# Kernel tuning notes

Measured on AMD Instinct MI355X. Metric: run time of the kernel, lower is better.

The kernel has to match this reference:

```python
import jax, jax.numpy as jnp
from jax import lax
import numpy as np

EPS = 0.15      # constraint_value_upper_bound (per-row box |y/c - 1| <= EPS)
DELTA = 0.05    # groups_constraint_upper_bound (per-group mean |y/c - 1| <= DELTA)
N_GROUPS = 8
N_ITERS = 300   # Dykstra iterations; converges to the exact QP projection

N, D, H1, H2, K = 65536, 512, 1024, 512, 1


def setup_inputs() -> dict:
    key = jax.random.key(0)
    ks = jax.random.split(key, 8)
    x = jax.random.normal(ks[0], (N, D), jnp.float32)
    W1 = jax.random.normal(ks[1], (D, H1), jnp.float32) / np.float32(np.sqrt(D))
    b1 = jnp.zeros((H1,), jnp.float32)
    W2 = jax.random.normal(ks[2], (H1, H2), jnp.float32) / np.float32(np.sqrt(H1))
    b2 = jnp.zeros((H2,), jnp.float32)
    Wf = jax.random.normal(ks[3], (H2, K), jnp.float32) / np.float32(np.sqrt(H2))
    bf = jnp.zeros((K,), jnp.float32)
    c = jax.random.uniform(ks[4], (N,), jnp.float32, 0.5, 2.0)
    # quantiles_price_tensor: q_i = (1/N) * #{k : c_k <= c_i}  (rank via searchsorted)
    q = jnp.searchsorted(jnp.sort(c), c, side='right').astype(jnp.float32) / N
    # group j covers q in [j/G, (j+1)/G]; assign boundary ties to the lower group
    g = jnp.clip(jnp.ceil(q * N_GROUPS).astype(jnp.int32) - 1, 0, N_GROUPS - 1)
    group_mask = jax.nn.one_hot(g, N_GROUPS, dtype=jnp.float32).T  # [G, N]
    return dict(x=x, W1=W1, b1=b1, W2=W2, b2=b2, Wf=Wf, bf=bf,
                constraint_constant=c, group_mask=group_mask)


def _project(y_u, c, group_mask):
    """Exact QP: min ||y - y_u||^2 s.t. |y_i/c_i - 1| <= EPS and
    |mean_{i in G_j}(y_i/c_i - 1)| <= DELTA, solved by Dykstra's alternating
    projections in z = y/c - 1 space under the weighted norm sum c_i^2 z_i^2."""
    w = c * c                                   # [N] weights of the norm
    z0 = y_u / c[:, None] - 1.0                 # [N, K]
    n = group_mask.sum(axis=1)                  # [G] group sizes
    a = group_mask / n[:, None]                 # [G, N] averaging rows
    denom = (a * a / w[None, :]).sum(axis=1)    # [G]  a^T W^{-1} a
    u = (a / w[None, :]) / denom[:, None]       # [G, N] weighted slab directions

    def proj_box(z):
        return jnp.clip(z, -EPS, EPS)

    def proj_grp(z):
        v = a @ z                               # [G, K] group means
        return z - u.T @ (v - jnp.clip(v, -DELTA, DELTA))

    def body(carry, _):
        z, p, q = carry
        zb = proj_box(z + p); p = z + p - zb
        zg = proj_grp(zb + q); q = zb + q - zg
        return (zg, p, q), None

    init = (z0, jnp.zeros_like(z0), jnp.zeros_like(z0))
    (z, _, _), _ = lax.scan(body, init, None, length=N_ITERS)
    return (z + 1.0) * c[:, None]


def reference(x, W1, b1, W2, b2, Wf, bf, constraint_constant, group_mask):
    h = jax.nn.relu(x @ W1 + b1)   # Dropout is identity in eval mode
    h = jax.nn.relu(h @ W2 + b2)
    y_u = h @ Wf + bf              # [N, 1] unconstrained predictions
    return _project(y_u, constraint_constant, group_mask)
```

## Files before the change

### kernel.cpp

```cpp
#include <hip/hip_runtime.h>
#include <hip/hip_bf16.h>

#define NROWS 65536
#define DIM   512
#define H1DIM 1024
#define H2DIM 512
#define EPSC  0.15f
#define DELTA 0.05f
#define NGRP  8
#define CAPG  16384

typedef __bf16 bf16x8 __attribute__((ext_vector_type(8)));
typedef float  f32x4  __attribute__((ext_vector_type(4)));

__device__ __forceinline__ void gload16(const void* g, void* lds) {
  __builtin_amdgcn_global_load_lds((__attribute__((address_space(1))) const unsigned int*)g,
                                   (__attribute__((address_space(3))) unsigned int*)lds,
                                   16, 0, 0);
}

__global__ void k_zero(float* y_u, int n, int* cnt) {
  int i = blockIdx.x * blockDim.x + threadIdx.x;
  if (i < n) y_u[i] = 0.f;
  if (i < NGRP) cnt[i] = 0;
}

__global__ void k_tcvt(const float* __restrict__ src, __bf16* __restrict__ dst, int R, int C) {
  __shared__ float tile[32][33];
  const int bi = blockIdx.x * 32;
  const int bj = blockIdx.y * 32;
  const int tx = threadIdx.x, ty = threadIdx.y;
  #pragma unroll
  for (int r = ty; r < 32; r += 8)
    tile[r][tx] = src[(size_t)(bi + r) * C + bj + tx];
  __syncthreads();
  #pragma unroll
  for (int r = ty; r < 32; r += 8)
    dst[(size_t)(bj + r) * R + bi + tx] = (__bf16)tile[tx][r];
}

__global__ __launch_bounds__(256) void k_cvt_x(const float4* __restrict__ x4,
                                               bf16x8* __restrict__ xb8, int n8) {
  int i = blockIdx.x * blockDim.x + threadIdx.x;
  const int stride = gridDim.x * blockDim.x;
  for (; i < n8; i += stride) {
    const float4 a = x4[2 * i];
    const float4 b = x4[2 * i + 1];
    bf16x8 v;
    v[0] = (__bf16)a.x; v[1] = (__bf16)a.y; v[2] = (__bf16)a.z; v[3] = (__bf16)a.w;
    v[4] = (__bf16)b.x; v[5] = (__bf16)b.y; v[6] = (__bf16)b.z; v[7] = (__bf16)b.w;
    xb8[i] = v;
  }
}


__global__ __launch_bounds__(512, 2) void k_gemm1(const __bf16* __restrict__ xb,
                                                  const __bf16* __restrict__ w1t,
                                                  const float* __restrict__ b1,
                                                  __bf16* __restrict__ h1) {
  __shared__ __align__(16) __bf16 As[2][256 * 64];
  __shared__ __align__(16) __bf16 Bs[2][256 * 64];
  const int tid = threadIdx.x;
  const int w = tid >> 6, l = tid & 63;
  const int mt   = (int)gridDim.x >> 2;
  const int mper = mt >> 3;
  const int xcd  = blockIdx.x & 7;
  const int idx  = blockIdx.x >> 3;
  const int brow = (xcd * mper + (idx >> 2)) * 256;
  const int bcol = (idx & 3) * 256;
  const int lr = l & 15, lk = l >> 4;
  const int wm = w >> 2, wn = w & 3;
  const int mbase = wm * 128, nbase = wn * 64;
  const int srow = w * 32 + (l >> 3);
  const int scol = (((l & 7) ^ ((l >> 3) & 7)) * 8);
  const int swz  = (lr & 7) << 4;
  const int NT = DIM / 64;
  f32x4 acc[8][4] = {};

  #define STAGE1(KT, BUF) do { \
    _Pragma("unroll") for (int t_ = 0; t_ < 4; ++t_) { \
      gload16(xb  + (size_t)(brow + srow + t_ * 8) * DIM + (KT) + scol, \
              As[BUF] + (w * 32 + t_ * 8) * 64); \
      gload16(w1t + (size_t)(bcol + srow + t_ * 8) * DIM + (KT) + scol, \
              Bs[BUF] + (w * 32 + t_ * 8) * 64); } } while (0)
  #define COMPUTE1(BUF) do { \
    _Pragma("unroll") for (int kk = 0; kk < 64; kk += 32) { \
      bf16x8 af[8], bq[4]; \
      _Pragma("unroll") for (int m = 0; m < 8; ++m) \
        af[m] = *(const bf16x8*)((const char*)(As[BUF]) + \
                 ((((mbase + m * 16 + lr) * 128) + kk * 2 + lk * 16) ^ swz)); \
      _Pragma("unroll") for (int nn = 0; nn < 4; ++nn) \
        bq[nn] = *(const bf16x8*)((const char*)(Bs[BUF]) + \
                 ((((nbase + nn * 16 + lr) * 128) + kk * 2 + lk * 16) ^ swz)); \
      __builtin_amdgcn_s_setprio(1); \
      _Pragma("unroll") for (int m = 0; m < 8; ++m) \
        _Pragma("unroll") for (int nn = 0; nn < 4; ++nn) \
          acc[m][nn] = __builtin_amdgcn_mfma_f32_16x16x32_bf16(af[m], bq[nn], acc[m][nn], 0, 0, 0); \
      __builtin_amdgcn_s_setprio(0); \
    } } while (0)

  STAGE1(0, 0);
  int cur = 0;
  for (int t = 0; t < NT - 1; ++t) {
    STAGE1((t + 1) * 64, cur ^ 1);
    asm volatile("s_waitcnt vmcnt(8)" ::: "memory");
    __builtin_amdgcn_s_barrier();
    COMPUTE1(cur);
    __builtin_amdgcn_s_barrier();
    cur ^= 1;
  }
  asm volatile("s_waitcnt vmcnt(0)" ::: "memory");
  __builtin_amdgcn_s_barrier();
  COMPUTE1(cur);

  #undef STAGE1
  #undef COMPUTE1

  #pragma unroll
  for (int nn = 0; nn < 4; ++nn) {
    const int col = bcol + nbase + nn * 16 + lr;
    const float bias = b1[col];
    #pragma unroll
    for (int m = 0; m < 8; ++m) {
      const int row = brow + mbase + m * 16 + lk * 4;
      #pragma unroll
      for (int j = 0; j < 4; ++j) {
        float v = acc[m][nn][j] + bias;
        v = fmaxf(v, 0.f);
        h1[(size_t)(row + j) * H1DIM + col] = (__bf16)v;
      }
    }
  }
}

__global__ __launch_bounds__(512, 2) void k_gemm2(const __bf16* __restrict__ h1,
                                                  const __bf16* __restrict__ w2t,
                                                  const float* __restrict__ b2,
                                                  const float* __restrict__ wf,
                                                  float* __restrict__ y_u, int row0) {
  __shared__ __align__(16) __bf16 As[2][256 * 64];
  __shared__ __align__(16) __bf16 Bs[2][256 * 64];
  __shared__ float yred[256];
  const int tid = threadIdx.x;
  const int w = tid >> 6, l = tid & 63;
  const int mt   = (int)gridDim.x >> 1;
  const int mper = mt >> 3;
  const int xcd  = blockIdx.x & 7;
  const int idx  = blockIdx.x >> 3;
  const int brow = (xcd * mper + (idx >> 1)) * 256;
  const int n0   = (idx & 1) * 256;
  const int lr = l & 15, lk = l >> 4;
  const int wm = w >> 2, wn = w & 3;
  const int mbase = wm * 128, nbase = wn * 64;
  const int srow = w * 32 + (l >> 3);
  const int scol = (((l & 7) ^ ((l >> 3) & 7)) * 8);
  const int swz  = (lr & 7) << 4;
  const int NT = H1DIM / 64;
  f32x4 acc[8][4] = {};

  #define STAGE2(KT, BUF) do { \
    _Pragma("unroll") for (int t_ = 0; t_ < 4; ++t_) { \
      gload16(h1  + (size_t)(brow + srow + t_ * 8) * H1DIM + (KT) + scol, \
              As[BUF] + (w * 32 + t_ * 8) * 64); \
      gload16(w2t + (size_t)(n0   + srow + t_ * 8) * H1DIM + (KT) + scol, \
              Bs[BUF] + (w * 32 + t_ * 8) * 64); } } while (0)
  #define COMPUTE2(BUF) do { \
    _Pragma("unroll") for (int kk = 0; kk < 64; kk += 32) { \
      bf16x8 af[8], bq[4]; \
      _Pragma("unroll") for (int m = 0; m < 8; ++m) \
        af[m] = *(const bf16x8*)((const char*)(As[BUF]) + \
                 ((((mbase + m * 16 + lr) * 128) + kk * 2 + lk * 16) ^ swz)); \
      _Pragma("unroll") for (int nn = 0; nn < 4; ++nn) \
        bq[nn] = *(const bf16x8*)((const char*)(Bs[BUF]) + \
                 ((((nbase + nn * 16 + lr) * 128) + kk * 2 + lk * 16) ^ swz)); \
      __builtin_amdgcn_s_setprio(1); \
      _Pragma("unroll") for (int m = 0; m < 8; ++m) \
        _Pragma("unroll") for (int nn = 0; nn < 4; ++nn) \
          acc[m][nn] = __builtin_amdgcn_mfma_f32_16x16x32_bf16(af[m], bq[nn], acc[m][nn], 0, 0, 0); \
      __builtin_amdgcn_s_setprio(0); \
    } } while (0)

  STAGE2(0, 0);
  int cur = 0;
  for (int t = 0; t < NT - 1; ++t) {
    STAGE2((t + 1) * 64, cur ^ 1);
    asm volatile("s_waitcnt vmcnt(8)" ::: "memory");
    __builtin_amdgcn_s_barrier();
    COMPUTE2(cur);
    __builtin_amdgcn_s_barrier();
    cur ^= 1;
  }
  asm volatile("s_waitcnt vmcnt(0)" ::: "memory");
  __builtin_amdgcn_s_barrier();
  COMPUTE2(cur);

  #undef STAGE2
  #undef COMPUTE2

  float yacc[8][4] = {};
  #pragma unroll
  for (int nn = 0; nn < 4; ++nn) {
    const int col = n0 + nbase + nn * 16 + lr;
    const float bias = b2[col];
    const float wfv = wf[col];
    #pragma unroll
    for (int m = 0; m < 8; ++m)
      #pragma unroll
      for (int j = 0; j < 4; ++j)
        yacc[m][j] += fmaxf(acc[m][nn][j] + bias, 0.f) * wfv;
  }
  #pragma unroll
  for (int m = 0; m < 8; ++m)
    #pragma unroll
    for (int j = 0; j < 4; ++j) {
      float v = yacc[m][j];
      v += __shfl_xor(v, 1, 64);
      v += __shfl_xor(v, 2, 64);
      v += __shfl_xor(v, 4, 64);
      v += __shfl_xor(v, 8, 64);
      yacc[m][j] = v;
    }
  if (tid < 256) yred[tid] = 0.f;
  __syncthreads();
  if (lr == 0) {
    #pragma unroll
    for (int m = 0; m < 8; ++m)
      #pragma unroll
      for (int j = 0; j < 4; ++j)
        atomicAdd(&yred[mbase + m * 16 + lk * 4 + j], yacc[m][j]);
  }
  __syncthreads();
  if (tid < 256) atomicAdd(&y_u[row0 + brow + tid], yred[tid]);
}

__global__ __launch_bounds__(256) void k_scatter(const float* __restrict__ y_u,
                                                 const float* __restrict__ c,
                                                 const float* __restrict__ mask,
                                                 const float* __restrict__ bfp,
                                                 float* __restrict__ z0c, float* __restrict__ wc,
                                                 unsigned char* __restrict__ gidx,
                                                 int* __restrict__ cnt, int n) {
  __shared__ int lcnt[NGRP];
  __shared__ int lbase[NGRP];
  const float bf0 = bfp[0];
  const int tid = threadIdx.x;
  if (tid < NGRP) lcnt[tid] = 0;
  __syncthreads();
  const int i = blockIdx.x * blockDim.x + tid;
  int g = 0, slot_l = 0;
  float z0 = 0.f, wv = 0.f;
  if (i < n) {
    const float cv = c[i];
    z0 = (y_u[i] + bf0) / cv - 1.f;
    wv = cv * cv;
    #pragma unroll
    for (int j = 1; j < NGRP; ++j)
      if (mask[(size_t)j * NROWS + i] > 0.5f) g = j;
    slot_l = atomicAdd(&lcnt[g], 1);
    gidx[i] = (unsigned char)g;
  }
  __syncthreads();
  if (tid < NGRP) lbase[tid] = atomicAdd(&cnt[tid], lcnt[tid]);
  __syncthreads();
  if (i < n) {
    const int slot = lbase[g] + slot_l;
    if (slot < CAPG) {
      z0c[(size_t)g * CAPG + slot] = z0;
      wc [(size_t)g * CAPG + slot] = wv;
    }
  }
}

__device__ __forceinline__ float wave_red(float v, int mode) {
  #pragma unroll
  for (int o = 32; o > 0; o >>= 1) {
    float u = __shfl_xor(v, o, 64);
    v = (mode == 0) ? (v + u) : ((mode == 1) ? fmaxf(v, u) : fminf(v, u));
  }
  return v;
}
__device__ __forceinline__ float block_red(float v, int mode, float* red, int tid) {
  v = wave_red(v, mode);
  if ((tid & 63) == 0) red[tid >> 6] = v;
  __syncthreads();
  if (tid < 64) {
    float x = (tid < 16) ? red[tid] : (mode == 0 ? 0.f : (mode == 1 ? -1e30f : 1e30f));
    x = wave_red(x, mode);
    if (tid == 0) red[0] = x;
  }
  __syncthreads();
  float r = red[0];
  __syncthreads();
  return r;
}

__global__ __launch_bounds__(1024) void k_mu(const float* __restrict__ z0c,
                                             const float* __restrict__ wc,
                                             const int* __restrict__ cnt,
                                             float* __restrict__ muarr) {
  __shared__ float red[16];
  const int g = blockIdx.x;
  const int tid = threadIdx.x;
  int n = cnt[g];
  if (n > CAPG) n = CAPG;
  if (n <= 0) { if (tid == 0) muarr[g] = 0.f; return; }
  float z0v[16], iwv[16];
  float hmax = -1e30f, hmin = 1e30f;
  #pragma unroll
  for (int t = 0; t < 16; ++t) {
    const int idx = t * 1024 + tid;
    if (idx < n) {
      const float z0 = z0c[(size_t)g * CAPG + idx];
      const float wv = wc[(size_t)g * CAPG + idx];
      z0v[t] = z0; iwv[t] = 1.f / wv;
      hmax = fmaxf(hmax, (z0 + EPSC) * wv);
      hmin = fminf(hmin, (z0 - EPSC) * wv);
    } else { z0v[t] = 0.f; iwv[t] = 0.f; }
  }
  const float inv_n = 1.f / (float)n;
  #define EVALM(MU, OUT) do { float s_ = 0.f; \
    _Pragma("unroll") for (int t = 0; t < 16; ++t) \
      s_ += fminf(fmaxf(z0v[t] - (MU) * iwv[t], -EPSC), EPSC); \
    OUT = block_red(s_, 0, red, tid) * inv_n; } while (0)
  float m0; EVALM(0.f, m0);
  float mu = 0.f;
  if (fabsf(m0) > DELTA) {
    float target, lo, hi;
    if (m0 > 0.f) { target = DELTA;  lo = 0.f; hi = block_red(hmax, 1, red, tid); }
    else          { target = -DELTA; hi = 0.f; lo = block_red(hmin, 2, red, tid); }
    for (int it = 0; it < 32; ++it) {
      const float mid = 0.5f * (lo + hi);
      float mm; EVALM(mid, mm);
      if (mm >= target) lo = mid; else hi = mid;
    }
    mu = 0.5f * (lo + hi);
  }
  if (tid == 0) muarr[g] = mu;
  #undef EVALM
}

__global__ void k_y(const float* __restrict__ y_u, const float* __restrict__ c,
                    const float* __restrict__ bfp, const unsigned char* __restrict__ gidx,
                    const float* __restrict__ muarr, float* __restrict__ out, int n) {
  const float bf0 = bfp[0];
  int i = blockIdx.x * blockDim.x + threadIdx.x;
  const int stride = gridDim.x * blockDim.x;
  for (; i < n; i += stride) {
    const float cv = c[i];
    const float z0 = (y_u[i] + bf0) / cv - 1.f;
    const float wv = cv * cv;
    const float mu = muarr[gidx[i]];
    const float z = fminf(fmaxf(z0 - mu / wv, -EPSC), EPSC);
    out[i] = (z + 1.f) * cv;
  }
}

extern "C" void kernel_launch(void* const* d_in, const int* in_sizes, int n_in,
                              void* d_out, int out_size, void* d_ws, size_t ws_size,
                              hipStream_t stream) {
  const float* x    = (const float*)d_in[0];
  const float* W1   = (const float*)d_in[1];
  const float* b1   = (const float*)d_in[2];
  const float* W2   = (const float*)d_in[3];
  const float* b2   = (const float*)d_in[4];
  const float* Wf   = (const float*)d_in[5];
  const float* bfp  = (const float*)d_in[6];
  const float* c    = (const float*)d_in[7];
  const float* mask = (const float*)d_in[8];
  float* out = (float*)d_out;

  char* ws = (char*)d_ws;
  size_t off = 0;
  auto alloc = [&](size_t bytes) -> void* {
    void* p = ws + off;
    off += (bytes + 255) & ~(size_t)255;
    return p;
  };
  __bf16* w1t = (__bf16*)alloc((size_t)H1DIM * DIM * 2);
  __bf16* w2t = (__bf16*)alloc((size_t)H2DIM * H1DIM * 2);
  float* y_u  = (float*)alloc((size_t)NROWS * 4);
  float* z0c  = (float*)alloc((size_t)NGRP * CAPG * 4);
  float* wc   = (float*)alloc((size_t)NGRP * CAPG * 4);
  unsigned char* gidx = (unsigned char*)alloc(NROWS);
  int*   cnt  = (int*)alloc(NGRP * 4);
  float* muarr = (float*)alloc(NGRP * 4);
  const size_t fixed = off;

  size_t avail = (ws_size > fixed) ? (ws_size - fixed) : 0;
  long long rc = (long long)(avail / ((size_t)(DIM + H1DIM * 2)));
  rc &= ~2047LL;
  if (rc > 32768) rc = 32768;
  if (rc < 2048) rc = 2048;
  const int rows_chunk = (int)rc;
  __bf16* xb = (__bf16*)(ws + fixed);
  __bf16* h1 = (__bf16*)(ws + fixed + (size_t)rows_chunk * DIM * 2);

  k_zero<<<dim3((NROWS + 255) / 256), dim3(256), 0, stream>>>(y_u, NROWS, cnt);
  k_tcvt<<<dim3(DIM / 32, H1DIM / 32), dim3(32, 8), 0, stream>>>(W1, w1t, DIM, H1DIM);
  k_tcvt<<<dim3(H1DIM / 32, H2DIM / 32), dim3(32, 8), 0, stream>>>(W2, w2t, H1DIM, H2DIM);

  for (int r0 = 0; r0 < NROWS; r0 += rows_chunk) {
    const int Mc = (NROWS - r0 < rows_chunk) ? (NROWS - r0) : rows_chunk;
    const int mtiles = Mc / 256;
    const int n8 = Mc * (DIM / 8);
    int cblocks = (n8 + 255) / 256; if (cblocks > 2048) cblocks = 2048;
    k_cvt_x<<<dim3(cblocks), dim3(256), 0, stream>>>(
        (const float4*)(x + (size_t)r0 * DIM), (bf16x8*)xb, n8);
    k_gemm1<<<dim3(mtiles * 4), dim3(512), 0, stream>>>(xb, w1t, b1, h1);
    k_gemm2<<<dim3(mtiles * 2), dim3(512), 0, stream>>>(h1, w2t, b2, Wf, y_u, r0);
  }

  k_scatter<<<dim3((NROWS + 255) / 256), dim3(256), 0, stream>>>(y_u, c, mask, bfp, z0c, wc, gidx, cnt, NROWS);
  k_mu<<<dim3(NGRP), dim3(1024), 0, stream>>>(z0c, wc, cnt, muarr);
  k_y<<<dim3(256), dim3(256), 0, stream>>>(y_u, c, bfp, gidx, muarr, out, NROWS);
}
```

Before: 242.0 us.

## Split GEMM k-tile compute into barrier-separated quadrant phases for LDS/MFMA interleave

Both GEMM kernels' per-k-tile compute is restructured into four quadrant phases: A and B fragments are read from LDS in halves and MFMAs run on 2x2 quadrants of the accumulator tile, with block barriers between phases. The goal is to stagger waves so that, with two blocks per CU, one wave's LDS reads overlap another's MFMA bursts, and to lower peak fragment-register pressure. In exchange it adds eight barriers per k-tile, which may serialize waves and add stall overhead. The loop is also restructured so the final tile runs inside the loop.

```diff
diff --git a/kernel.cpp b/kernel.cpp
--- a/kernel.cpp
+++ b/kernel.cpp
@@ -53,6 +53,44 @@
   }
 }
 
+
+#define RD_A(LDSA, MH) do { \
+  _Pragma("unroll") for (int kk_ = 0; kk_ < 2; ++kk_) \
+    _Pragma("unroll") for (int m_ = 0; m_ < 4; ++m_) \
+      aR[kk_][m_] = *(const bf16x8*)((const char*)(LDSA) + \
+        ((((mbase + (MH) * 64 + m_ * 16 + lr) * 128) + kk_ * 64 + lk * 16) ^ swz)); \
+} while (0)
+#define RD_B(LDSB, NH) do { \
+  _Pragma("unroll") for (int kk_ = 0; kk_ < 2; ++kk_) \
+    _Pragma("unroll") for (int j_ = 0; j_ < 2; ++j_) \
+      bR[NH][kk_][j_] = *(const bf16x8*)((const char*)(LDSB) + \
+        ((((nbase + (NH) * 32 + j_ * 16 + lr) * 128) + kk_ * 64 + lk * 16) ^ swz)); \
+} while (0)
+#define MFMA_Q(MH, NH) do { \
+  __builtin_amdgcn_s_setprio(1); \
+  _Pragma("unroll") for (int kk_ = 0; kk_ < 2; ++kk_) \
+    _Pragma("unroll") for (int m_ = 0; m_ < 4; ++m_) \
+      _Pragma("unroll") for (int j_ = 0; j_ < 2; ++j_) \
+        acc[(MH) * 4 + m_][(NH) * 2 + j_] = __builtin_amdgcn_mfma_f32_16x16x32_bf16( \
+            aR[kk_][m_], bR[NH][kk_][j_], acc[(MH) * 4 + m_][(NH) * 2 + j_], 0, 0, 0); \
+  __builtin_amdgcn_s_setprio(0); \
+} while (0)
+#define KTILE_PHASES(BUFA, BUFB) do { \
+  RD_A(BUFA, 0); RD_B(BUFB, 0); \
+  __builtin_amdgcn_s_barrier(); \
+  MFMA_Q(0, 0); \
+  __builtin_amdgcn_s_barrier(); \
+  RD_B(BUFB, 1); \
+  __builtin_amdgcn_s_barrier(); \
+  MFMA_Q(0, 1); \
+  __builtin_amdgcn_s_barrier(); \
+  RD_A(BUFA, 1); \
+  __builtin_amdgcn_s_barrier(); \
+  MFMA_Q(1, 1); \
+  __builtin_amdgcn_s_barrier(); \
+  MFMA_Q(1, 0); \
+  __builtin_amdgcn_s_barrier(); \
+} while (0)
 
 __global__ __launch_bounds__(512, 2) void k_gemm1(const __bf16* __restrict__ xb,
                                                   const __bf16* __restrict__ w1t,
@@ -76,6 +114,8 @@
   const int swz  = (lr & 7) << 4;
   const int NT = DIM / 64;
   f32x4 acc[8][4] = {};
+  bf16x8 aR[2][4];
+  bf16x8 bR[2][2][2];
 
   #define STAGE1(KT, BUF) do { \
     _Pragma("unroll") for (int t_ = 0; t_ < 4; ++t_) { \
@@ -83,38 +123,21 @@
               As[BUF] + (w * 32 + t_ * 8) * 64); \
       gload16(w1t + (size_t)(bcol + srow + t_ * 8) * DIM + (KT) + scol, \
               Bs[BUF] + (w * 32 + t_ * 8) * 64); } } while (0)
-  #define COMPUTE1(BUF) do { \
-    _Pragma("unroll") for (int kk = 0; kk < 64; kk += 32) { \
-      bf16x8 af[8], bq[4]; \
-      _Pragma("unroll") for (int m = 0; m < 8; ++m) \
-        af[m] = *(const bf16x8*)((const char*)(As[BUF]) + \
-                 ((((mbase + m * 16 + lr) * 128) + kk * 2 + lk * 16) ^ swz)); \
-      _Pragma("unroll") for (int nn = 0; nn < 4; ++nn) \
-        bq[nn] = *(const bf16x8*)((const char*)(Bs[BUF]) + \
-                 ((((nbase + nn * 16 + lr) * 128) + kk * 2 + lk * 16) ^ swz)); \
-      __builtin_amdgcn_s_setprio(1); \
-      _Pragma("unroll") for (int m = 0; m < 8; ++m) \
-        _Pragma("unroll") for (int nn = 0; nn < 4; ++nn) \
-          acc[m][nn] = __builtin_amdgcn_mfma_f32_16x16x32_bf16(af[m], bq[nn], acc[m][nn], 0, 0, 0); \
-      __builtin_amdgcn_s_setprio(0); \
-    } } while (0)
 
   STAGE1(0, 0);
   int cur = 0;
-  for (int t = 0; t < NT - 1; ++t) {
-    STAGE1((t + 1) * 64, cur ^ 1);
-    asm volatile("s_waitcnt vmcnt(8)" ::: "memory");
+  for (int t = 0; t < NT; ++t) {
+    if (t + 1 < NT) {
+      STAGE1((t + 1) * 64, cur ^ 1);
+      asm volatile("s_waitcnt vmcnt(8)" ::: "memory");
+    } else {
+      asm volatile("s_waitcnt vmcnt(0)" ::: "memory");
+    }
     __builtin_amdgcn_s_barrier();
-    COMPUTE1(cur);
-    __builtin_amdgcn_s_barrier();
+    KTILE_PHASES(As[cur], Bs[cur]);
     cur ^= 1;
   }
-  asm volatile("s_waitcnt vmcnt(0)" ::: "memory");
-  __builtin_amdgcn_s_barrier();
-  COMPUTE1(cur);
-
   #undef STAGE1
-  #undef COMPUTE1
 
   #pragma unroll
   for (int nn = 0; nn < 4; ++nn) {
@@ -157,6 +180,8 @@
   const int swz  = (lr & 7) << 4;
   const int NT = H1DIM / 64;
   f32x4 acc[8][4] = {};
+  bf16x8 aR[2][4];
+  bf16x8 bR[2][2][2];
 
   #define STAGE2(KT, BUF) do { \
     _Pragma("unroll") for (int t_ = 0; t_ < 4; ++t_) { \
@@ -164,38 +189,21 @@
               As[BUF] + (w * 32 + t_ * 8) * 64); \
       gload16(w2t + (size_t)(n0   + srow + t_ * 8) * H1DIM + (KT) + scol, \
               Bs[BUF] + (w * 32 + t_ * 8) * 64); } } while (0)
-  #define COMPUTE2(BUF) do { \
-    _Pragma("unroll") for (int kk = 0; kk < 64; kk += 32) { \
-      bf16x8 af[8], bq[4]; \
-      _Pragma("unroll") for (int m = 0; m < 8; ++m) \
-        af[m] = *(const bf16x8*)((const char*)(As[BUF]) + \
-                 ((((mbase + m * 16 + lr) * 128) + kk * 2 + lk * 16) ^ swz)); \
-      _Pragma("unroll") for (int nn = 0; nn < 4; ++nn) \
-        bq[nn] = *(const bf16x8*)((const char*)(Bs[BUF]) + \
-                 ((((nbase + nn * 16 + lr) * 128) + kk * 2 + lk * 16) ^ swz)); \
-      __builtin_amdgcn_s_setprio(1); \
-      _Pragma("unroll") for (int m = 0; m < 8; ++m) \
-        _Pragma("unroll") for (int nn = 0; nn < 4; ++nn) \
-          acc[m][nn] = __builtin_amdgcn_mfma_f32_16x16x32_bf16(af[m], bq[nn], acc[m][nn], 0, 0, 0); \
-      __builtin_amdgcn_s_setprio(0); \
-    } } while (0)
 
   STAGE2(0, 0);
   int cur = 0;
-  for (int t = 0; t < NT - 1; ++t) {
-    STAGE2((t + 1) * 64, cur ^ 1);
-    asm volatile("s_waitcnt vmcnt(8)" ::: "memory");
+  for (int t = 0; t < NT; ++t) {
+    if (t + 1 < NT) {
+      STAGE2((t + 1) * 64, cur ^ 1);
+      asm volatile("s_waitcnt vmcnt(8)" ::: "memory");
+    } else {
+      asm volatile("s_waitcnt vmcnt(0)" ::: "memory");
+    }
     __builtin_amdgcn_s_barrier();
-    COMPUTE2(cur);
-    __builtin_amdgcn_s_barrier();
+    KTILE_PHASES(As[cur], Bs[cur]);
     cur ^= 1;
   }
-  asm volatile("s_waitcnt vmcnt(0)" ::: "memory");
-  __builtin_amdgcn_s_barrier();
-  COMPUTE2(cur);
-
   #undef STAGE2
-  #undef COMPUTE2
 
   float yacc[8][4] = {};
   #pragma unroll
```

After: 256.1 us. 5.9% more time.

## Fuse projection tail into one per-group kernel with Newton-bisection solve

Applied to the files above, without the earlier changes.

Replaces the scatter, mu-solve and output kernels with a single per-group kernel. It compacts each group's rows into LDS with a ballot-based scan, solves for the group's dual multiplier with a safeguarded Newton step in 12 iterations instead of 32 bisection steps, and writes the outputs directly. The y_u zeroing moves into the first conversion kernel, which removes one more launch. The cost is a serial read of the full mask row by only 8 blocks, plus an LDS capacity cap of 10240 rows per group.

```diff
diff --git a/kernel.cpp b/kernel.cpp
--- a/kernel.cpp
+++ b/kernel.cpp
@@ -8,7 +8,7 @@
 #define EPSC  0.15f
 #define DELTA 0.05f
 #define NGRP  8
-#define CAPG  16384
+#define PCAP  10240
 
 typedef __bf16 bf16x8 __attribute__((ext_vector_type(8)));
 typedef float  f32x4  __attribute__((ext_vector_type(4)));
@@ -17,12 +17,6 @@
   __builtin_amdgcn_global_load_lds((__attribute__((address_space(1))) const unsigned int*)g,
                                    (__attribute__((address_space(3))) unsigned int*)lds,
                                    16, 0, 0);
-}
-
-__global__ void k_zero(float* y_u, int n, int* cnt) {
-  int i = blockIdx.x * blockDim.x + threadIdx.x;
-  if (i < n) y_u[i] = 0.f;
-  if (i < NGRP) cnt[i] = 0;
 }
 
 __global__ void k_tcvt(const float* __restrict__ src, __bf16* __restrict__ dst, int R, int C) {
@@ -40,10 +34,10 @@
 }
 
 __global__ __launch_bounds__(256) void k_cvt_x(const float4* __restrict__ x4,
-                                               bf16x8* __restrict__ xb8, int n8) {
-  int i = blockIdx.x * blockDim.x + threadIdx.x;
+                                               bf16x8* __restrict__ xb8, int n8,
+                                               float* __restrict__ y_u, int zn) {
   const int stride = gridDim.x * blockDim.x;
-  for (; i < n8; i += stride) {
+  for (int i = blockIdx.x * blockDim.x + threadIdx.x; i < n8; i += stride) {
     const float4 a = x4[2 * i];
     const float4 b = x4[2 * i + 1];
     bf16x8 v;
@@ -51,6 +45,8 @@
     v[4] = (__bf16)b.x; v[5] = (__bf16)b.y; v[6] = (__bf16)b.z; v[7] = (__bf16)b.w;
     xb8[i] = v;
   }
+  for (int j = blockIdx.x * blockDim.x + threadIdx.x; j < zn; j += stride)
+    y_u[j] = 0.f;
 }
 
 
@@ -233,126 +229,134 @@
   if (tid < 256) atomicAdd(&y_u[row0 + brow + tid], yred[tid]);
 }
 
-__global__ __launch_bounds__(256) void k_scatter(const float* __restrict__ y_u,
-                                                 const float* __restrict__ c,
-                                                 const float* __restrict__ mask,
-                                                 const float* __restrict__ bfp,
-                                                 float* __restrict__ z0c, float* __restrict__ wc,
-                                                 unsigned char* __restrict__ gidx,
-                                                 int* __restrict__ cnt, int n) {
-  __shared__ int lcnt[NGRP];
-  __shared__ int lbase[NGRP];
-  const float bf0 = bfp[0];
-  const int tid = threadIdx.x;
-  if (tid < NGRP) lcnt[tid] = 0;
-  __syncthreads();
-  const int i = blockIdx.x * blockDim.x + tid;
-  int g = 0, slot_l = 0;
-  float z0 = 0.f, wv = 0.f;
-  if (i < n) {
-    const float cv = c[i];
-    z0 = (y_u[i] + bf0) / cv - 1.f;
-    wv = cv * cv;
-    #pragma unroll
-    for (int j = 1; j < NGRP; ++j)
-      if (mask[(size_t)j * NROWS + i] > 0.5f) g = j;
-    slot_l = atomicAdd(&lcnt[g], 1);
-    gidx[i] = (unsigned char)g;
-  }
-  __syncthreads();
-  if (tid < NGRP) lbase[tid] = atomicAdd(&cnt[tid], lcnt[tid]);
-  __syncthreads();
-  if (i < n) {
-    const int slot = lbase[g] + slot_l;
-    if (slot < CAPG) {
-      z0c[(size_t)g * CAPG + slot] = z0;
-      wc [(size_t)g * CAPG + slot] = wv;
-    }
-  }
-}
-
-__device__ __forceinline__ float wave_red(float v, int mode) {
-  #pragma unroll
-  for (int o = 32; o > 0; o >>= 1) {
-    float u = __shfl_xor(v, o, 64);
-    v = (mode == 0) ? (v + u) : ((mode == 1) ? fmaxf(v, u) : fminf(v, u));
-  }
-  return v;
-}
-__device__ __forceinline__ float block_red(float v, int mode, float* red, int tid) {
-  v = wave_red(v, mode);
-  if ((tid & 63) == 0) red[tid >> 6] = v;
-  __syncthreads();
-  if (tid < 64) {
-    float x = (tid < 16) ? red[tid] : (mode == 0 ? 0.f : (mode == 1 ? -1e30f : 1e30f));
-    x = wave_red(x, mode);
-    if (tid == 0) red[0] = x;
-  }
-  __syncthreads();
-  float r = red[0];
-  __syncthreads();
-  return r;
-}
-
-__global__ __launch_bounds__(1024) void k_mu(const float* __restrict__ z0c,
-                                             const float* __restrict__ wc,
-                                             const int* __restrict__ cnt,
-                                             float* __restrict__ muarr) {
-  __shared__ float red[16];
+__global__ __launch_bounds__(1024) void k_proj(const float* __restrict__ y_u,
+                                               const float* __restrict__ c,
+                                               const float* __restrict__ mask,
+                                               const float* __restrict__ bfp,
+                                               float* __restrict__ out) {
+  __shared__ float z0s[PCAP];
+  __shared__ float iws[PCAP];
+  __shared__ int   idxs[PCAP];
+  __shared__ float reds[16], redd[16];
+  __shared__ int   gcount;
   const int g = blockIdx.x;
   const int tid = threadIdx.x;
-  int n = cnt[g];
-  if (n > CAPG) n = CAPG;
-  if (n <= 0) { if (tid == 0) muarr[g] = 0.f; return; }
-  float z0v[16], iwv[16];
+  const int lane = tid & 63;
+  const int wid = tid >> 6;
+  const float bf0 = bfp[0];
+  if (tid == 0) gcount = 0;
+  __syncthreads();
+  for (int i = tid; i < NROWS; i += 1024) {
+    const bool in = mask[(size_t)g * NROWS + i] > 0.5f;
+    const unsigned long long b = __ballot(in);
+    const int pre = __popcll(b & ((1ull << lane) - 1));
+    int wbase = 0;
+    if (lane == 0 && b) wbase = atomicAdd(&gcount, __popcll(b));
+    wbase = __shfl(wbase, 0, 64);
+    if (in) {
+      const int s = wbase + pre;
+      if (s < PCAP) {
+        const float cv = c[i];
+        z0s[s]  = (y_u[i] + bf0) / cv - 1.f;
+        iws[s]  = 1.f / (cv * cv);
+        idxs[s] = i;
+      }
+    }
+  }
+  __syncthreads();
+  int n = gcount; if (n > PCAP) n = PCAP;
+  const float inv_n = (n > 0) ? 1.f / (float)n : 0.f;
+  float z0v[10], iwv[10];
   float hmax = -1e30f, hmin = 1e30f;
   #pragma unroll
-  for (int t = 0; t < 16; ++t) {
-    const int idx = t * 1024 + tid;
-    if (idx < n) {
-      const float z0 = z0c[(size_t)g * CAPG + idx];
-      const float wv = wc[(size_t)g * CAPG + idx];
-      z0v[t] = z0; iwv[t] = 1.f / wv;
-      hmax = fmaxf(hmax, (z0 + EPSC) * wv);
-      hmin = fminf(hmin, (z0 - EPSC) * wv);
+  for (int t = 0; t < 10; ++t) {
+    const int s = t * 1024 + tid;
+    if (s < n) {
+      z0v[t] = z0s[s]; iwv[t] = iws[s];
+      const float wv = 1.f / iwv[t];
+      hmax = fmaxf(hmax, (z0v[t] + EPSC) * wv);
+      hmin = fminf(hmin, (z0v[t] - EPSC) * wv);
     } else { z0v[t] = 0.f; iwv[t] = 0.f; }
   }
-  const float inv_n = 1.f / (float)n;
-  #define EVALM(MU, OUT) do { float s_ = 0.f; \
-    _Pragma("unroll") for (int t = 0; t < 16; ++t) \
-      s_ += fminf(fmaxf(z0v[t] - (MU) * iwv[t], -EPSC), EPSC); \
-    OUT = block_red(s_, 0, red, tid) * inv_n; } while (0)
-  float m0; EVALM(0.f, m0);
+  #define RED2(SV, DV) do { \
+    _Pragma("unroll") for (int o_ = 32; o_ > 0; o_ >>= 1) { \
+      SV += __shfl_xor(SV, o_, 64); DV += __shfl_xor(DV, o_, 64); } \
+    if (lane == 0) { reds[wid] = SV; redd[wid] = DV; } \
+    __syncthreads(); \
+    if (tid < 64) { \
+      float a_ = (tid < 16) ? reds[tid] : 0.f; \
+      float b_ = (tid < 16) ? redd[tid] : 0.f; \
+      _Pragma("unroll") for (int o_ = 32; o_ > 0; o_ >>= 1) { \
+        a_ += __shfl_xor(a_, o_, 64); b_ += __shfl_xor(b_, o_, 64); } \
+      if (tid == 0) { reds[0] = a_; redd[0] = b_; } \
+    } \
+    __syncthreads(); \
+    SV = reds[0]; DV = redd[0]; \
+    __syncthreads(); \
+  } while (0)
+  #define EVAL2(MU, MS, DS) do { \
+    float s_ = 0.f, d_ = 0.f; \
+    _Pragma("unroll") for (int t_ = 0; t_ < 10; ++t_) { \
+      float zz_ = z0v[t_] - (MU) * iwv[t_]; \
+      if (zz_ > EPSC) zz_ = EPSC; \
+      else if (zz_ < -EPSC) zz_ = -EPSC; \
+      else d_ += iwv[t_]; \
+      s_ += zz_; } \
+    RED2(s_, d_); \
+    MS = s_ * inv_n; DS = d_ * inv_n; \
+  } while (0)
   float mu = 0.f;
-  if (fabsf(m0) > DELTA) {
-    float target, lo, hi;
-    if (m0 > 0.f) { target = DELTA;  lo = 0.f; hi = block_red(hmax, 1, red, tid); }
-    else          { target = -DELTA; hi = 0.f; lo = block_red(hmin, 2, red, tid); }
-    for (int it = 0; it < 32; ++it) {
-      const float mid = 0.5f * (lo + hi);
-      float mm; EVALM(mid, mm);
-      if (mm >= target) lo = mid; else hi = mid;
+  if (n > 0) {
+    float m0, d0;
+    EVAL2(0.f, m0, d0);
+    if (fabsf(m0) > DELTA) {
+      float hx = hmax, hn = -hmin;
+      #pragma unroll
+      for (int o_ = 32; o_ > 0; o_ >>= 1) {
+        hx = fmaxf(hx, __shfl_xor(hx, o_, 64));
+        hn = fmaxf(hn, __shfl_xor(hn, o_, 64));
+      }
+      if (lane == 0) { reds[wid] = hx; redd[wid] = hn; }
+      __syncthreads();
+      if (tid < 64) {
+        float a_ = (tid < 16) ? reds[tid] : -1e30f;
+        float b_ = (tid < 16) ? redd[tid] : -1e30f;
+        #pragma unroll
+        for (int o_ = 32; o_ > 0; o_ >>= 1) {
+          a_ = fmaxf(a_, __shfl_xor(a_, o_, 64));
+          b_ = fmaxf(b_, __shfl_xor(b_, o_, 64));
+        }
+        if (tid == 0) { reds[0] = a_; redd[0] = b_; }
+      }
+      __syncthreads();
+      const float hmax_r = reds[0], hmin_r = -redd[0];
+      __syncthreads();
+      float target, lo, hi;
+      if (m0 > 0.f) { target = DELTA;  lo = 0.f;     hi = hmax_r; }
+      else          { target = -DELTA; lo = hmin_r;  hi = 0.f;    }
+      mu = 0.5f * (lo + hi);
+      for (int it = 0; it < 12; ++it) {
+        float mm, dd;
+        EVAL2(mu, mm, dd);
+        if (mm >= target) lo = mu; else hi = mu;
+        float nm = (dd > 0.f) ? mu + (mm - target) / dd : 0.5f * (lo + hi);
+        if (!(nm > lo && nm < hi)) nm = 0.5f * (lo + hi);
+        mu = nm;
+      }
     }
-    mu = 0.5f * (lo + hi);
-  }
-  if (tid == 0) muarr[g] = mu;
-  #undef EVALM
-}
-
-__global__ void k_y(const float* __restrict__ y_u, const float* __restrict__ c,
-                    const float* __restrict__ bfp, const unsigned char* __restrict__ gidx,
-                    const float* __restrict__ muarr, float* __restrict__ out, int n) {
-  const float bf0 = bfp[0];
-  int i = blockIdx.x * blockDim.x + threadIdx.x;
-  const int stride = gridDim.x * blockDim.x;
-  for (; i < n; i += stride) {
-    const float cv = c[i];
-    const float z0 = (y_u[i] + bf0) / cv - 1.f;
-    const float wv = cv * cv;
-    const float mu = muarr[gidx[i]];
-    const float z = fminf(fmaxf(z0 - mu / wv, -EPSC), EPSC);
-    out[i] = (z + 1.f) * cv;
-  }
+  }
+  #pragma unroll
+  for (int t = 0; t < 10; ++t) {
+    const int s = t * 1024 + tid;
+    if (s < n) {
+      float z = z0v[t] - mu * iwv[t];
+      z = fminf(fmaxf(z, -EPSC), EPSC);
+      const int ri = idxs[s];
+      out[ri] = (z + 1.f) * c[ri];
+    }
+  }
+  #undef RED2
+  #undef EVAL2
 }
 
 extern "C" void kernel_launch(void* const* d_in, const int* in_sizes, int n_in,
@@ -379,15 +383,10 @@
   __bf16* w1t = (__bf16*)alloc((size_t)H1DIM * DIM * 2);
   __bf16* w2t = (__bf16*)alloc((size_t)H2DIM * H1DIM * 2);
   float* y_u  = (float*)alloc((size_t)NROWS * 4);
-  float* z0c  = (float*)alloc((size_t)NGRP * CAPG * 4);
-  float* wc   = (float*)alloc((size_t)NGRP * CAPG * 4);
-  unsigned char* gidx = (unsigned char*)alloc(NROWS);
-  int*   cnt  = (int*)alloc(NGRP * 4);
-  float* muarr = (float*)alloc(NGRP * 4);
   const size_t fixed = off;
 
   size_t avail = (ws_size > fixed) ? (ws_size - fixed) : 0;
-  long long rc = (long long)(avail / ((size_t)(DIM + H1DIM * 2)));
+  long long rc = (long long)(avail / ((size_t)(DIM * 2 + H1DIM * 2)));
   rc &= ~2047LL;
   if (rc > 32768) rc = 32768;
   if (rc < 2048) rc = 2048;
@@ -395,22 +394,22 @@
   __bf16* xb = (__bf16*)(ws + fixed);
   __bf16* h1 = (__bf16*)(ws + fixed + (size_t)rows_chunk * DIM * 2);
 
-  k_zero<<<dim3((NROWS + 255) / 256), dim3(256), 0, stream>>>(y_u, NROWS, cnt);
   k_tcvt<<<dim3(DIM / 32, H1DIM / 32), dim3(32, 8), 0, stream>>>(W1, w1t, DIM, H1DIM);
   k_tcvt<<<dim3(H1DIM / 32, H2DIM / 32), dim3(32, 8), 0, stream>>>(W2, w2t, H1DIM, H2DIM);
 
+  bool first = true;
   for (int r0 = 0; r0 < NROWS; r0 += rows_chunk) {
     const int Mc = (NROWS - r0 < rows_chunk) ? (NROWS - r0) : rows_chunk;
     const int mtiles = Mc / 256;
     const int n8 = Mc * (DIM / 8);
     int cblocks = (n8 + 255) / 256; if (cblocks > 2048) cblocks = 2048;
     k_cvt_x<<<dim3(cblocks), dim3(256), 0, stream>>>(
-        (const float4*)(x + (size_t)r0 * DIM), (bf16x8*)xb, n8);
+        (const float4*)(x + (size_t)r0 * DIM), (bf16x8*)xb, n8,
+        y_u, first ? NROWS : 0);
+    first = false;
     k_gemm1<<<dim3(mtiles * 4), dim3(512), 0, stream>>>(xb, w1t, b1, h1);
     k_gemm2<<<dim3(mtiles * 2), dim3(512), 0, stream>>>(h1, w2t, b2, Wf, y_u, r0);
   }
 
-  k_scatter<<<dim3((NROWS + 255) / 256), dim3(256), 0, stream>>>(y_u, c, mask, bfp, z0c, wc, gidx, cnt, NROWS);
-  k_mu<<<dim3(NGRP), dim3(1024), 0, stream>>>(z0c, wc, cnt, muarr);
-  k_y<<<dim3(256), dim3(256), 0, stream>>>(y_u, c, bfp, gidx, muarr, out, NROWS);
-}
+  k_proj<<<dim3(NGRP), dim3(1024), 0, stream>>>(y_u, c, mask, bfp, out);
+}
```

After: 279.9 us. 15.7% more time.

## Replace bisection for group multiplier with safeguarded Newton and fuse zero-init

Applied to the files above, without the earlier changes.

The per-group dual multiplier search in k_mu drops 32 bisection steps in favour of about 12 safeguarded Newton steps. Each step reduces the clipped sum and its derivative (the sum of inverse weights over unclipped entries) together in one paired block reduction, and the two max/min bound reductions are merged into one pass. This is meant to cut the serial chain of block-wide reductions and barriers in a kernel that runs only 8 blocks. The separate zeroing kernel is folded into the first k_cvt_x launch, and inverse weights are stored precomputed. The workspace chunk sizing formula also changes, which may give fewer, smaller row chunks, and Newton accuracy relies on the bisection fallback.

```diff
diff --git a/kernel.cpp b/kernel.cpp
--- a/kernel.cpp
+++ b/kernel.cpp
@@ -19,12 +19,6 @@
                                    16, 0, 0);
 }
 
-__global__ void k_zero(float* y_u, int n, int* cnt) {
-  int i = blockIdx.x * blockDim.x + threadIdx.x;
-  if (i < n) y_u[i] = 0.f;
-  if (i < NGRP) cnt[i] = 0;
-}
-
 __global__ void k_tcvt(const float* __restrict__ src, __bf16* __restrict__ dst, int R, int C) {
   __shared__ float tile[32][33];
   const int bi = blockIdx.x * 32;
@@ -40,10 +34,12 @@
 }
 
 __global__ __launch_bounds__(256) void k_cvt_x(const float4* __restrict__ x4,
-                                               bf16x8* __restrict__ xb8, int n8) {
-  int i = blockIdx.x * blockDim.x + threadIdx.x;
+                                               bf16x8* __restrict__ xb8, int n8,
+                                               float* __restrict__ y_u, int zn,
+                                               int* __restrict__ cnt) {
   const int stride = gridDim.x * blockDim.x;
-  for (; i < n8; i += stride) {
+  const int tid0 = blockIdx.x * blockDim.x + threadIdx.x;
+  for (int i = tid0; i < n8; i += stride) {
     const float4 a = x4[2 * i];
     const float4 b = x4[2 * i + 1];
     bf16x8 v;
@@ -51,6 +47,8 @@
     v[4] = (__bf16)b.x; v[5] = (__bf16)b.y; v[6] = (__bf16)b.z; v[7] = (__bf16)b.w;
     xb8[i] = v;
   }
+  for (int j = tid0; j < zn; j += stride) y_u[j] = 0.f;
+  if (zn > 0 && tid0 < NGRP) cnt[tid0] = 0;
 }
 
 
@@ -237,7 +235,7 @@
                                                  const float* __restrict__ c,
                                                  const float* __restrict__ mask,
                                                  const float* __restrict__ bfp,
-                                                 float* __restrict__ z0c, float* __restrict__ wc,
+                                                 float* __restrict__ z0c, float* __restrict__ iwc,
                                                  unsigned char* __restrict__ gidx,
                                                  int* __restrict__ cnt, int n) {
   __shared__ int lcnt[NGRP];
@@ -248,11 +246,11 @@
   __syncthreads();
   const int i = blockIdx.x * blockDim.x + tid;
   int g = 0, slot_l = 0;
-  float z0 = 0.f, wv = 0.f;
+  float z0 = 0.f, iw = 0.f;
   if (i < n) {
     const float cv = c[i];
     z0 = (y_u[i] + bf0) / cv - 1.f;
-    wv = cv * cv;
+    iw = 1.f / (cv * cv);
     #pragma unroll
     for (int j = 1; j < NGRP; ++j)
       if (mask[(size_t)j * NROWS + i] > 0.5f) g = j;
@@ -266,39 +264,39 @@
     const int slot = lbase[g] + slot_l;
     if (slot < CAPG) {
       z0c[(size_t)g * CAPG + slot] = z0;
-      wc [(size_t)g * CAPG + slot] = wv;
-    }
-  }
-}
-
-__device__ __forceinline__ float wave_red(float v, int mode) {
+      iwc[(size_t)g * CAPG + slot] = iw;
+    }
+  }
+}
+
+__device__ __forceinline__ void red2(float& a, float& b, float* reda, float* redb, int tid) {
   #pragma unroll
   for (int o = 32; o > 0; o >>= 1) {
-    float u = __shfl_xor(v, o, 64);
-    v = (mode == 0) ? (v + u) : ((mode == 1) ? fmaxf(v, u) : fminf(v, u));
-  }
-  return v;
-}
-__device__ __forceinline__ float block_red(float v, int mode, float* red, int tid) {
-  v = wave_red(v, mode);
-  if ((tid & 63) == 0) red[tid >> 6] = v;
+    a += __shfl_xor(a, o, 64);
+    b += __shfl_xor(b, o, 64);
+  }
+  if ((tid & 63) == 0) { reda[tid >> 6] = a; redb[tid >> 6] = b; }
   __syncthreads();
   if (tid < 64) {
-    float x = (tid < 16) ? red[tid] : (mode == 0 ? 0.f : (mode == 1 ? -1e30f : 1e30f));
-    x = wave_red(x, mode);
-    if (tid == 0) red[0] = x;
-  }
-  __syncthreads();
-  float r = red[0];
-  __syncthreads();
-  return r;
+    float x = (tid < 16) ? reda[tid] : 0.f;
+    float y = (tid < 16) ? redb[tid] : 0.f;
+    #pragma unroll
+    for (int o = 32; o > 0; o >>= 1) {
+      x += __shfl_xor(x, o, 64);
+      y += __shfl_xor(y, o, 64);
+    }
+    if (tid == 0) { reda[0] = x; redb[0] = y; }
+  }
+  __syncthreads();
+  a = reda[0]; b = redb[0];
+  __syncthreads();
 }
 
 __global__ __launch_bounds__(1024) void k_mu(const float* __restrict__ z0c,
-                                             const float* __restrict__ wc,
+                                             const float* __restrict__ iwc,
                                              const int* __restrict__ cnt,
                                              float* __restrict__ muarr) {
-  __shared__ float red[16];
+  __shared__ float reda[16], redb[16];
   const int g = blockIdx.x;
   const int tid = threadIdx.x;
   int n = cnt[g];
@@ -311,32 +309,66 @@
     const int idx = t * 1024 + tid;
     if (idx < n) {
       const float z0 = z0c[(size_t)g * CAPG + idx];
-      const float wv = wc[(size_t)g * CAPG + idx];
-      z0v[t] = z0; iwv[t] = 1.f / wv;
+      const float iw = iwc[(size_t)g * CAPG + idx];
+      z0v[t] = z0; iwv[t] = iw;
+      const float wv = 1.f / iw;
       hmax = fmaxf(hmax, (z0 + EPSC) * wv);
       hmin = fminf(hmin, (z0 - EPSC) * wv);
     } else { z0v[t] = 0.f; iwv[t] = 0.f; }
   }
   const float inv_n = 1.f / (float)n;
-  #define EVALM(MU, OUT) do { float s_ = 0.f; \
-    _Pragma("unroll") for (int t = 0; t < 16; ++t) \
-      s_ += fminf(fmaxf(z0v[t] - (MU) * iwv[t], -EPSC), EPSC); \
-    OUT = block_red(s_, 0, red, tid) * inv_n; } while (0)
-  float m0; EVALM(0.f, m0);
+  #define EVAL2(MU, MS, DS) do { \
+    float s_ = 0.f, d_ = 0.f; \
+    _Pragma("unroll") for (int t_ = 0; t_ < 16; ++t_) { \
+      float zz_ = z0v[t_] - (MU) * iwv[t_]; \
+      if (zz_ > EPSC) zz_ = EPSC; \
+      else if (zz_ < -EPSC) zz_ = -EPSC; \
+      else d_ += iwv[t_]; \
+      s_ += zz_; } \
+    red2(s_, d_, reda, redb, tid); \
+    MS = s_ * inv_n; DS = d_ * inv_n; \
+  } while (0)
+  float m0, d0;
+  EVAL2(0.f, m0, d0);
   float mu = 0.f;
   if (fabsf(m0) > DELTA) {
+    float hx = hmax, hn = -hmin;
+    #pragma unroll
+    for (int o = 32; o > 0; o >>= 1) {
+      hx = fmaxf(hx, __shfl_xor(hx, o, 64));
+      hn = fmaxf(hn, __shfl_xor(hn, o, 64));
+    }
+    if ((tid & 63) == 0) { reda[tid >> 6] = hx; redb[tid >> 6] = hn; }
+    __syncthreads();
+    if (tid < 64) {
+      float x = (tid < 16) ? reda[tid] : -1e30f;
+      float y = (tid < 16) ? redb[tid] : -1e30f;
+      #pragma unroll
+      for (int o = 32; o > 0; o >>= 1) {
+        x = fmaxf(x, __shfl_xor(x, o, 64));
+        y = fmaxf(y, __shfl_xor(y, o, 64));
+      }
+      if (tid == 0) { reda[0] = x; redb[0] = y; }
+    }
+    __syncthreads();
+    const float hmax_r = reda[0], hmin_r = -redb[0];
+    __syncthreads();
     float target, lo, hi;
-    if (m0 > 0.f) { target = DELTA;  lo = 0.f; hi = block_red(hmax, 1, red, tid); }
-    else          { target = -DELTA; hi = 0.f; lo = block_red(hmin, 2, red, tid); }
-    for (int it = 0; it < 32; ++it) {
-      const float mid = 0.5f * (lo + hi);
-      float mm; EVALM(mid, mm);
-      if (mm >= target) lo = mid; else hi = mid;
-    }
-    mu = 0.5f * (lo + hi);
+    if (m0 > 0.f) { target = DELTA;  lo = 0.f;    hi = hmax_r; }
+    else          { target = -DELTA; lo = hmin_r; hi = 0.f;    }
+    mu = (d0 > 0.f) ? (m0 - target) / d0 : 0.5f * (lo + hi);
+    if (!(mu > lo && mu < hi)) mu = 0.5f * (lo + hi);
+    for (int it = 0; it < 12; ++it) {
+      float mm, dd;
+      EVAL2(mu, mm, dd);
+      if (mm >= target) lo = mu; else hi = mu;
+      float nm = (dd > 0.f) ? mu + (mm - target) / dd : 0.5f * (lo + hi);
+      if (!(nm > lo && nm < hi)) nm = 0.5f * (lo + hi);
+      mu = nm;
+    }
   }
   if (tid == 0) muarr[g] = mu;
-  #undef EVALM
+  #undef EVAL2
 }
 
 __global__ void k_y(const float* __restrict__ y_u, const float* __restrict__ c,
@@ -348,9 +380,8 @@
   for (; i < n; i += stride) {
     const float cv = c[i];
     const float z0 = (y_u[i] + bf0) / cv - 1.f;
-    const float wv = cv * cv;
     const float mu = muarr[gidx[i]];
-    const float z = fminf(fmaxf(z0 - mu / wv, -EPSC), EPSC);
+    const float z = fminf(fmaxf(z0 - mu / (cv * cv), -EPSC), EPSC);
     out[i] = (z + 1.f) * cv;
   }
 }
@@ -380,14 +411,14 @@
   __bf16* w2t = (__bf16*)alloc((size_t)H2DIM * H1DIM * 2);
   float* y_u  = (float*)alloc((size_t)NROWS * 4);
   float* z0c  = (float*)alloc((size_t)NGRP * CAPG * 4);
-  float* wc   = (float*)alloc((size_t)NGRP * CAPG * 4);
+  float* iwc  = (float*)alloc((size_t)NGRP * CAPG * 4);
   unsigned char* gidx = (unsigned char*)alloc(NROWS);
   int*   cnt  = (int*)alloc(NGRP * 4);
   float* muarr = (float*)alloc(NGRP * 4);
   const size_t fixed = off;
 
   size_t avail = (ws_size > fixed) ? (ws_size - fixed) : 0;
-  long long rc = (long long)(avail / ((size_t)(DIM + H1DIM * 2)));
+  long long rc = (long long)(avail / ((size_t)(DIM * 2 + H1DIM * 2)));
   rc &= ~2047LL;
   if (rc > 32768) rc = 32768;
   if (rc < 2048) rc = 2048;
@@ -395,22 +426,24 @@
   __bf16* xb = (__bf16*)(ws + fixed);
   __bf16* h1 = (__bf16*)(ws + fixed + (size_t)rows_chunk * DIM * 2);
 
-  k_zero<<<dim3((NROWS + 255) / 256), dim3(256), 0, stream>>>(y_u, NROWS, cnt);
   k_tcvt<<<dim3(DIM / 32, H1DIM / 32), dim3(32, 8), 0, stream>>>(W1, w1t, DIM, H1DIM);
   k_tcvt<<<dim3(H1DIM / 32, H2DIM / 32), dim3(32, 8), 0, stream>>>(W2, w2t, H1DIM, H2DIM);
 
+  bool first = true;
   for (int r0 = 0; r0 < NROWS; r0 += rows_chunk) {
     const int Mc = (NROWS - r0 < rows_chunk) ? (NROWS - r0) : rows_chunk;
     const int mtiles = Mc / 256;
     const int n8 = Mc * (DIM / 8);
     int cblocks = (n8 + 255) / 256; if (cblocks > 2048) cblocks = 2048;
     k_cvt_x<<<dim3(cblocks), dim3(256), 0, stream>>>(
-        (const float4*)(x + (size_t)r0 * DIM), (bf16x8*)xb, n8);
+        (const float4*)(x + (size_t)r0 * DIM), (bf16x8*)xb, n8,
+        y_u, first ? NROWS : 0, cnt);
+    first = false;
     k_gemm1<<<dim3(mtiles * 4), dim3(512), 0, stream>>>(xb, w1t, b1, h1);
     k_gemm2<<<dim3(mtiles * 2), dim3(512), 0, stream>>>(h1, w2t, b2, Wf, y_u, r0);
   }
 
-  k_scatter<<<dim3((NROWS + 255) / 256), dim3(256), 0, stream>>>(y_u, c, mask, bfp, z0c, wc, gidx, cnt, NROWS);
-  k_mu<<<dim3(NGRP), dim3(1024), 0, stream>>>(z0c, wc, cnt, muarr);
+  k_scatter<<<dim3((NROWS + 255) / 256), dim3(256), 0, stream>>>(y_u, c, mask, bfp, z0c, iwc, gidx, cnt, NROWS);
+  k_mu<<<dim3(NGRP), dim3(1024), 0, stream>>>(z0c, iwc, cnt, muarr);
   k_y<<<dim3(256), dim3(256), 0, stream>>>(y_u, c, bfp, gidx, muarr, out, NROWS);
 }
```

Result: faster. 231.7 us (-4.2%).
